# Kernel tuning notes

Hardware: AMD Instinct MI355X
Metric: run time of the kernel (lower is better)

## Reference

```python
import jax, jax.numpy as jnp
import numpy as np

B = 32768; SLOTS = 8; HEADS = 4; HEAD = 32; KEY = 32
MEM = HEADS * HEAD          # 128
QKV = 2 * KEY + HEAD        # 96 per head
TOT = HEADS * QKV           # 384
NGATE = 2 * MEM             # 256 (input + forget, unit gating)
FORGET_BIAS = 1.0; INPUT_BIAS = 0.0


def _ln(x, g, b, eps=1e-5):
    m = jnp.mean(x, axis=-1, keepdims=True)
    v = jnp.var(x, axis=-1, keepdims=True)
    return g * (x - m) * jax.lax.rsqrt(v + eps) + b


def setup_inputs():
    ks = jax.random.split(jax.random.key(0), 10)
    n = lambda k, shape, s=0.05: jax.random.normal(k, shape, dtype=jnp.float32) * s
    return {
        'inputs': jax.random.normal(ks[0], (B, MEM), dtype=jnp.float32),
        'memory': jax.random.normal(ks[1], (B, SLOTS, MEM), dtype=jnp.float32),
        'W_in': n(ks[2], (MEM, MEM)), 'b_in': jnp.zeros((MEM,), jnp.float32),
        'W_qkv': n(ks[3], (MEM, TOT)), 'b_qkv': jnp.zeros((TOT,), jnp.float32),
        'ln_qkv_g': jnp.ones((TOT,), jnp.float32), 'ln_qkv_b': jnp.zeros((TOT,), jnp.float32),
        'ln1_g': jnp.ones((MEM,), jnp.float32), 'ln1_b': jnp.zeros((MEM,), jnp.float32),
        'W_m1': n(ks[4], (MEM, MEM)), 'b_m1': jnp.zeros((MEM,), jnp.float32),
        'W_m2': n(ks[5], (MEM, MEM)), 'b_m2': jnp.zeros((MEM,), jnp.float32),
        'ln2_g': jnp.ones((MEM,), jnp.float32), 'ln2_b': jnp.zeros((MEM,), jnp.float32),
        'W_gi': n(ks[6], (MEM, NGATE)), 'b_gi': jnp.zeros((NGATE,), jnp.float32),
        'W_gm': n(ks[7], (MEM, NGATE)), 'b_gm': jnp.zeros((NGATE,), jnp.float32),
    }


def _forward(inputs, memory, W_in, b_in, W_qkv, b_qkv, ln_qkv_g, ln_qkv_b,
             ln1_g, ln1_b, W_m1, b_m1, W_m2, b_m2, ln2_g, ln2_b,
             W_gi, b_gi, W_gm, b_gm):
    x = inputs @ W_in + b_in                                  # [B, MEM]
    mp = jnp.concatenate([memory, x[:, None, :]], axis=1)     # [B, S1, MEM]
    S1 = SLOTS + 1
    # --- attend over memory (num_blocks = 1) ---
    qkv = _ln(mp @ W_qkv + b_qkv, ln_qkv_g, ln_qkv_b)         # [B, S1, TOT]
    qkv = qkv.reshape(-1, S1, HEADS, QKV).transpose(0, 2, 1, 3)  # [B, H, S1, QKV]
    q = qkv[..., :KEY] * (QKV ** -0.5)   # note: source scales by qkv_size, not key_size
    k = qkv[..., KEY:2 * KEY]
    v = qkv[..., 2 * KEY:]
    attn = jax.nn.softmax(jnp.einsum('bhqd,bhkd->bhqk', q, k), axis=-1)
    out = jnp.einsum('bhqk,bhkd->bhqd', attn, v)
    out = out.transpose(0, 2, 1, 3).reshape(-1, S1, MEM)      # [B, S1, MEM]
    mem = _ln(mp + out, ln1_g, ln1_b)
    mlp = (mem @ W_m1 + b_m1) @ W_m2 + b_m2   # stacked linears, no nonlinearity (as in source)
    mem = _ln(mlp + mem, ln2_g, ln2_b)
    next_mem = mem[:, :-1, :]                                 # drop input slot -> [B, SLOTS, MEM]
    # --- LSTM-style unit gating ---
    gi = x @ W_gi + b_gi                                      # [B, NGATE]
    gm = jnp.tanh(memory) @ W_gm + b_gm                       # [B, SLOTS, NGATE]
    gates = gm + gi[:, None, :]
    input_gate = jax.nn.sigmoid(gates[..., :MEM] + INPUT_BIAS)
    forget_gate = jax.nn.sigmoid(gates[..., MEM:] + FORGET_BIAS)
    next_mem = input_gate * jnp.tanh(next_mem) + forget_gate * memory
    output = next_mem.reshape(next_mem.shape[0], -1)          # [B, SLOTS*MEM]
    return output, next_mem


def reference(inputs, memory, W_in, b_in, W_qkv, b_qkv, ln_qkv_g, ln_qkv_b,
              ln1_g, ln1_b, W_m1, b_m1, W_m2, b_m2, ln2_g, ln2_b,
              W_gi, b_gi, W_gm, b_gm):
    return _forward(inputs, memory, W_in, b_in, W_qkv, b_qkv, ln_qkv_g, ln_qkv_b,
                    ln1_g, ln1_b, W_m1, b_m1, W_m2, b_m2, ln2_g, ln2_b,
                    W_gi, b_gi, W_gm, b_gm)
```

## Files before the change

kernel.cpp:

```cpp
#include <hip/hip_runtime.h>
#include <cstdint>
#include <cstddef>

#define BATCH   32768
#define BT      4
#define S1      9
#define RROWS   36
#define NBLK    (BATCH/BT)

#define WS_WIN   0
#define WS_WQKV  32768
#define WS_WC    131072
#define WS_WGI   163840
#define WS_WGM   229376
#define WS_BC    294912

#define A_OFF  27648
#define X_OFF  36864
#define MEM2   19456
#define LDSSZ  37888

typedef __bf16 bf16x8 __attribute__((ext_vector_type(8), may_alias));
typedef __bf16 bf16x4 __attribute__((ext_vector_type(4), may_alias));
typedef float  f32x4  __attribute__((ext_vector_type(4), may_alias));
typedef __bf16 bf16s  __attribute__((may_alias));
typedef float  f32s   __attribute__((may_alias));

__device__ __forceinline__ float sigmoidf_(float x){ return 1.f/(1.f+__expf(-x)); }
__device__ __forceinline__ float tanhf_(float x){ float e = __expf(2.f*x); return 1.f - 2.f/(e+1.f); }

__device__ __forceinline__ char* swz(char* base, int row, int stride, int colb){
  return base + row*stride + (colb ^ ((row & 7) << 4));
}

__global__ __launch_bounds__(256) void prep_kernel(
    const float* __restrict__ W_in,  const float* __restrict__ W_qkv,
    const float* __restrict__ W_m1,  const float* __restrict__ W_m2,
    const float* __restrict__ b_m1,  const float* __restrict__ b_m2,
    const float* __restrict__ W_gi,  const float* __restrict__ W_gm,
    __bf16* __restrict__ ws, float* __restrict__ bc)
{
  int gt = blockIdx.x*256 + threadIdx.x;
  int NT = gridDim.x*256;
  for (int i = gt; i < 128*128; i += NT){ int n=i>>7, k=i&127; ws[(WS_WIN >>1)+i] = (__bf16)W_in [k*128+n]; }
  for (int i = gt; i < 384*128; i += NT){ int n=i>>7, k=i&127; ws[(WS_WQKV>>1)+i] = (__bf16)W_qkv[k*384+n]; }
  for (int i = gt; i < 256*128; i += NT){ int n=i>>7, k=i&127; ws[(WS_WGI >>1)+i] = (__bf16)W_gi [k*256+n]; }
  for (int i = gt; i < 256*128; i += NT){ int n=i>>7, k=i&127; ws[(WS_WGM >>1)+i] = (__bf16)W_gm [k*256+n]; }
  for (int i = gt; i < 128*128; i += NT){
    int n=i>>7, k=i&127;
    float s = 0.f;
    for (int j=0;j<128;j++) s += W_m1[k*128+j]*W_m2[j*128+n];
    ws[(WS_WC>>1)+i] = (__bf16)s;
  }
  for (int i = gt; i < 128; i += NT){
    float s = b_m2[i];
    for (int j=0;j<128;j++) s += b_m1[j]*W_m2[j*128+i];
    bc[i] = s;
  }
}

__global__ __launch_bounds__(256, 4) void rmc_kernel(
    const float* __restrict__ inputs, const float* __restrict__ memory,
    const float* __restrict__ b_in,   const float* __restrict__ b_qkv,
    const float* __restrict__ lnq_g,  const float* __restrict__ lnq_b,
    const float* __restrict__ ln1_g,  const float* __restrict__ ln1_b,
    const float* __restrict__ ln2_g,  const float* __restrict__ ln2_b,
    const float* __restrict__ b_gi,   const float* __restrict__ b_gm,
    const __bf16* __restrict__ wWin,  const __bf16* __restrict__ wWqkv,
    const __bf16* __restrict__ wWc,   const __bf16* __restrict__ wWgi,
    const __bf16* __restrict__ wWgm,  const float* __restrict__ bc,
    float* __restrict__ out0, float* __restrict__ out1)
{
  __shared__ __align__(16) char smem[LDSSZ];
  char* Q = smem;
  char* A = smem + A_OFF;
  char* X = smem + X_OFF;

  const int tid  = threadIdx.x;
  const int lane = tid & 63;
  const int wv   = tid >> 6;
  const int l15  = lane & 15;
  const int lg   = lane >> 4;
  const int b0   = blockIdx.x * BT;
  const float QSC = 0.1020620726159658f;

  if (tid < 64){
    int r = tid >> 4, c = tid & 15;
    const float* gp = inputs + (size_t)(b0+r)*128 + c*8;
    f32x4 a = *(const f32x4*)gp, b = *(const f32x4*)(gp+4);
    bf16x8 h;
    h[0]=(__bf16)a[0]; h[1]=(__bf16)a[1]; h[2]=(__bf16)a[2]; h[3]=(__bf16)a[3];
    h[4]=(__bf16)b[0]; h[5]=(__bf16)b[1]; h[6]=(__bf16)b[2]; h[7]=(__bf16)b[3];
    *(bf16x8*)swz(X, r, 256, c*16) = h;
  }
  for (int t = tid; t < 512; t += 256){
    int r = t >> 4, c8 = (t & 15)*8;
    const float* gp = memory + (size_t)(b0 + (r>>3))*1024 + (r&7)*128 + c8;
    f32x4 a = *(const f32x4*)gp, b = *(const f32x4*)(gp+4);
    bf16x8 h;
    h[0]=(__bf16)a[0]; h[1]=(__bf16)a[1]; h[2]=(__bf16)a[2]; h[3]=(__bf16)a[3];
    h[4]=(__bf16)b[0]; h[5]=(__bf16)b[1]; h[6]=(__bf16)b[2]; h[7]=(__bf16)b[3];
    *(bf16x8*)swz(A, (r>>3)*S1 + (r&7), 256, c8*2) = h;
  }
  __syncthreads();

  {
    const int xr = (l15 < BT) ? l15 : (BT-1);
    bf16x8 aX[4];
#pragma unroll
    for (int k=0;k<4;k++) aX[k] = *(const bf16x8*)swz(X, xr, 256, k*64 + lg*16);
    f32x4 accX[2];
#pragma unroll
    for (int n=0;n<2;n++){
      int nt = wv*2 + n;
      f32x4 acc = {0.f,0.f,0.f,0.f};
#pragma unroll
      for (int k=0;k<4;k++){
        bf16x8 b = *(const bf16x8*)(wWin + (nt*16 + l15)*128 + k*32 + 8*lg);
        acc = __builtin_amdgcn_mfma_f32_16x16x32_bf16(aX[k], b, acc, 0, 0, 0);
      }
      accX[n] = acc;
    }
    __syncthreads();
#pragma unroll
    for (int n=0;n<2;n++){
#pragma unroll
      for (int r=0;r<4;r++){
        int row = 4*lg + r;
        if (row < BT){
          int col = (wv*2+n)*16 + l15;
          __bf16 h = (__bf16)(accX[n][r] + b_in[col]);
          *(bf16s*)swz(X, row, 256, col*2) = h;
          *(bf16s*)swz(A, row*S1+8, 256, col*2) = h;
        }
      }
    }
  }
  __syncthreads();

  {
    bf16x8 aQ[3][4];
#pragma unroll
    for (int m=0;m<3;m++){
      int ar = m*16 + l15; ar = (ar < RROWS) ? ar : (RROWS-1);
#pragma unroll
      for (int k=0;k<4;k++)
        aQ[m][k] = *(const bf16x8*)swz(A, ar, 256, k*64 + lg*16);
    }
#pragma unroll
    for (int half=0; half<2; ++half){
      f32x4 accQ[3][3];
#pragma unroll
      for (int m=0;m<3;m++)
#pragma unroll
        for (int n=0;n<3;n++) accQ[m][n] = (f32x4){0.f,0.f,0.f,0.f};
#pragma unroll
      for (int n=0;n<3;n++){
        int nt = wv*6 + half*3 + n;
#pragma unroll
        for (int k=0;k<4;k++){
          bf16x8 b = *(const bf16x8*)(wWqkv + (nt*16 + l15)*128 + k*32 + 8*lg);
#pragma unroll
          for (int m=0;m<3;m++)
            accQ[m][n] = __builtin_amdgcn_mfma_f32_16x16x32_bf16(aQ[m][k], b, accQ[m][n], 0, 0, 0);
        }
      }
#pragma unroll
      for (int m=0;m<3;m++)
#pragma unroll
        for (int n=0;n<3;n++)
#pragma unroll
          for (int r=0;r<4;r++){
            int row = m*16 + 4*lg + r;
            if (row < RROWS){
              int col = (wv*6 + half*3 + n)*16 + l15;
              *(bf16s*)swz(Q, row, 768, col*2) = (__bf16)(accQ[m][n][r] + b_qkv[col]);
            }
          }
    }
  }
  __syncthreads();

  {
    float gq[6], bq[6];
#pragma unroll
    for (int t=0;t<6;t++){ gq[t] = lnq_g[lane+64*t]; bq[t] = lnq_b[lane+64*t]; }
    for (int r = wv; r < RROWS; r += 4){
      float x[6]; float s = 0.f, sq = 0.f;
#pragma unroll
      for (int t=0;t<6;t++){
        x[t] = (float)*(const bf16s*)swz(Q, r, 768, (lane + 64*t)*2);
        s += x[t]; sq += x[t]*x[t];
      }
#pragma unroll
      for (int o=1;o<64;o<<=1){ s += __shfl_xor(s,o); sq += __shfl_xor(sq,o); }
      float mean = s * (1.f/384.f);
      float var  = sq * (1.f/384.f) - mean*mean;
      float rs   = rsqrtf(var + 1e-5f);
#pragma unroll
      for (int t=0;t<6;t++){
        int c = lane + 64*t;
        float y = gq[t]*(x[t]-mean)*rs + bq[t];
        if ((c % 96) < 32) y *= QSC;
        *(bf16s*)swz(Q, r, 768, c*2) = (__bf16)y;
      }
    }
  }
  __syncthreads();

  {
    const int s = wv;
    const int arow = (l15 < 9) ? l15 : 8;
    f32x4 sc[4];
#pragma unroll
    for (int h=0;h<4;h++){
      bf16x8 qa = *(const bf16x8*)swz(Q, s*S1+arow, 768, h*192 + lg*16);
      bf16x8 kb = *(const bf16x8*)swz(Q, s*S1+arow, 768, h*192 + 64 + lg*16);
      sc[h] = __builtin_amdgcn_mfma_f32_16x16x32_bf16(qa, kb, (f32x4){0.f,0.f,0.f,0.f}, 0, 0, 0);
    }
#pragma unroll
    for (int h=0;h<4;h++){
#pragma unroll
      for (int r=0;r<4;r++){
        int row = 4*lg + r;
        float v = (l15 < 9) ? sc[h][r] : -1e30f;
        float mx = v;
#pragma unroll
        for (int o=1;o<16;o<<=1) mx = fmaxf(mx, __shfl_xor(mx, o));
        float p = __expf(v - mx);
        float sm = p;
#pragma unroll
        for (int o=1;o<16;o<<=1) sm += __shfl_xor(sm, o);
        float pn = p / sm;
        if (row < 9 && l15 < 9)
          *(f32s*)swz(Q, s*S1+row, 768, h*192 + l15*4) = pn;
      }
    }
  }
  __syncthreads();

#pragma unroll
  for (int pass=0; pass<3; ++pass){
    int ct = pass*256 + tid;
    float o8[8] = {0.f,0.f,0.f,0.f,0.f,0.f,0.f,0.f};
    int s=0, h=0, q=0, d16=0;
    if (ct < 576){
      s = ct/144; int r2 = ct%144;
      h = r2/36;  int r3 = r2%36;
      q = r3>>2;  d16 = (r3&3)*16;
      int cb = h*192;
#pragma unroll
      for (int k=0;k<9;k++){
        float p = *(const f32s*)swz(Q, s*S1+q, 768, cb + k*4);
        bf16x8 v8 = *(const bf16x8*)swz(Q, s*S1+k, 768, cb + 128 + d16);
#pragma unroll
        for (int e=0;e<8;e++) o8[e] += p*(float)v8[e];
      }
    }
    __syncthreads();
    if (ct < 576){
      bf16x8 ho;
#pragma unroll
      for (int e=0;e<8;e++) ho[e] = (__bf16)o8[e];
      *(bf16x8*)swz(Q, s*S1+q, 768, h*192 + d16) = ho;
    }
    __syncthreads();
  }

  {
    float g0 = ln1_g[lane], g1 = ln1_g[lane+64], e0 = ln1_b[lane], e1 = ln1_b[lane+64];
    const int ob0 = (lane>>5)*192 + (lane&31)*2;
    const int ob1 = ((lane>>5)+2)*192 + (lane&31)*2;
    for (int r = wv; r < RROWS; r += 4){
      float t0 = (float)*(const bf16s*)swz(A, r, 256, lane*2)
               + (float)*(const bf16s*)swz(Q, r, 768, ob0);
      float t1 = (float)*(const bf16s*)swz(A, r, 256, (lane+64)*2)
               + (float)*(const bf16s*)swz(Q, r, 768, ob1);
      float s = t0+t1, sq = t0*t0 + t1*t1;
#pragma unroll
      for (int o=1;o<64;o<<=1){ s += __shfl_xor(s,o); sq += __shfl_xor(sq,o); }
      float mean = s*(1.f/128.f), var = sq*(1.f/128.f) - mean*mean;
      float rs = rsqrtf(var + 1e-5f);
      *(bf16s*)swz(A, r, 256, lane*2)      = (__bf16)(g0*(t0-mean)*rs + e0);
      *(bf16s*)swz(A, r, 256, (lane+64)*2) = (__bf16)(g1*(t1-mean)*rs + e1);
    }
  }
  __syncthreads();

  {
    bf16x8 aM[3][4];
#pragma unroll
    for (int m=0;m<3;m++){
      int ar = m*16 + l15; ar = (ar < RROWS) ? ar : (RROWS-1);
#pragma unroll
      for (int k=0;k<4;k++)
        aM[m][k] = *(const bf16x8*)swz(A, ar, 256, k*64 + lg*16);
    }
    f32x4 accM[3][2];
#pragma unroll
    for (int m=0;m<3;m++)
#pragma unroll
      for (int n=0;n<2;n++) accM[m][n] = (f32x4){0.f,0.f,0.f,0.f};
#pragma unroll
    for (int n=0;n<2;n++){
      int nt = wv*2 + n;
#pragma unroll
      for (int k=0;k<4;k++){
        bf16x8 b = *(const bf16x8*)(wWc + (nt*16 + l15)*128 + k*32 + 8*lg);
#pragma unroll
        for (int m=0;m<3;m++)
          accM[m][n] = __builtin_amdgcn_mfma_f32_16x16x32_bf16(aM[m][k], b, accM[m][n], 0, 0, 0);
      }
    }
    __syncthreads();
#pragma unroll
    for (int m=0;m<3;m++)
#pragma unroll
      for (int n=0;n<2;n++)
#pragma unroll
        for (int r=0;r<4;r++){
          int row = m*16 + 4*lg + r;
          if (row < RROWS){
            int col = (wv*2+n)*16 + l15;
            *(f32s*)swz(Q, row, 512, col*4) = accM[m][n][r] + bc[col];
          }
        }
  }
  __syncthreads();

  {
    float g0 = ln2_g[lane], g1 = ln2_g[lane+64], e0 = ln2_b[lane], e1 = ln2_b[lane+64];
    for (int r = wv; r < RROWS; r += 4){
      if ((r % S1) == 8) continue;
      float t0 = *(const f32s*)swz(Q, r, 512, lane*4)
               + (float)*(const bf16s*)swz(A, r, 256, lane*2);
      float t1 = *(const f32s*)swz(Q, r, 512, (lane+64)*4)
               + (float)*(const bf16s*)swz(A, r, 256, (lane+64)*2);
      float s = t0+t1, sq = t0*t0 + t1*t1;
#pragma unroll
      for (int o=1;o<64;o<<=1){ s += __shfl_xor(s,o); sq += __shfl_xor(sq,o); }
      float mean = s*(1.f/128.f), var = sq*(1.f/128.f) - mean*mean;
      float rs = rsqrtf(var + 1e-5f);
      int rp = (r/S1)*8 + (r%S1);
      *(bf16s*)swz(Q + MEM2, rp, 256, lane*2)      = (__bf16)(g0*(t0-mean)*rs + e0);
      *(bf16s*)swz(Q + MEM2, rp, 256, (lane+64)*2) = (__bf16)(g1*(t1-mean)*rs + e1);
    }
  }
  __syncthreads();

  {
    const int xr = (l15 < BT) ? l15 : (BT-1);
    bf16x8 aG[4];
#pragma unroll
    for (int k=0;k<4;k++) aG[k] = *(const bf16x8*)swz(X, xr, 256, k*64 + lg*16);
    f32x4 accG[4];
#pragma unroll
    for (int n=0;n<4;n++) accG[n] = (f32x4){0.f,0.f,0.f,0.f};
#pragma unroll
    for (int n=0;n<4;n++){
      int nt = wv*4 + n;
#pragma unroll
      for (int k=0;k<4;k++){
        bf16x8 b = *(const bf16x8*)(wWgi + (nt*16 + l15)*128 + k*32 + 8*lg);
        accG[n] = __builtin_amdgcn_mfma_f32_16x16x32_bf16(aG[k], b, accG[n], 0, 0, 0);
      }
    }
#pragma unroll
    for (int n=0;n<4;n++)
#pragma unroll
      for (int r=0;r<4;r++){
        int row = 4*lg + r;
        if (row < BT){
          int col = (wv*4+n)*16 + l15;
          *(f32s*)swz(Q, row, 1024, col*4) = accG[n][r] + b_gi[col];
        }
      }
    for (int t = tid; t < 512; t += 256){
      int r = t >> 4, c8 = (t & 15)*8;
      const float* gp = memory + (size_t)(b0 + (r>>3))*1024 + (r&7)*128 + c8;
      f32x4 a = *(const f32x4*)gp, b = *(const f32x4*)(gp+4);
      bf16x8 h;
      h[0]=(__bf16)tanhf_(a[0]); h[1]=(__bf16)tanhf_(a[1]);
      h[2]=(__bf16)tanhf_(a[2]); h[3]=(__bf16)tanhf_(a[3]);
      h[4]=(__bf16)tanhf_(b[0]); h[5]=(__bf16)tanhf_(b[1]);
      h[6]=(__bf16)tanhf_(b[2]); h[7]=(__bf16)tanhf_(b[3]);
      *(bf16x8*)swz(A, r, 256, c8*2) = h;
    }
  }
  __syncthreads();

  {
#pragma unroll
    for (int m=0;m<2;m++){
      bf16x8 aT[4];
#pragma unroll
      for (int k=0;k<4;k++)
        aT[k] = *(const bf16x8*)swz(A, m*16 + l15, 256, k*64 + lg*16);
#pragma unroll
      for (int p=0;p<2;p++){
        f32x4 ai = {0.f,0.f,0.f,0.f}, af = {0.f,0.f,0.f,0.f};
        int ntI = 2*wv + p, ntF = 8 + 2*wv + p;
#pragma unroll
        for (int k=0;k<4;k++){
          bf16x8 bI = *(const bf16x8*)(wWgm + (ntI*16 + l15)*128 + k*32 + 8*lg);
          bf16x8 bF = *(const bf16x8*)(wWgm + (ntF*16 + l15)*128 + k*32 + 8*lg);
          ai = __builtin_amdgcn_mfma_f32_16x16x32_bf16(aT[k], bI, ai, 0, 0, 0);
          af = __builtin_amdgcn_mfma_f32_16x16x32_bf16(aT[k], bF, af, 0, 0, 0);
        }
        int c = wv*32 + p*16 + l15;
        float giv = *(const f32s*)swz(Q, 0, 1024, 0) * 0.f;
        giv = *(const f32s*)swz(Q, 0, 1024, c*4);
        float bgi = b_gm[c], bgf = b_gm[128+c];
#pragma unroll
        for (int r=0;r<4;r++){
          int row = m*16 + 4*lg + r;
          int s = row>>3, j = row&7;
          float g_i = ai[r] + bgi + *(const f32s*)swz(Q, s, 1024, c*4);
          float g_f = af[r] + bgf + *(const f32s*)swz(Q, s, 1024, (128+c)*4) + 1.0f;
          float ig = sigmoidf_(g_i), fg = sigmoidf_(g_f);
          float m2 = (float)*(const bf16s*)swz(Q + MEM2, row, 256, c*2);
          float mo = memory[(size_t)(b0+s)*1024 + j*128 + c];
          float nm = ig*tanhf_(m2) + fg*mo;
          size_t o = (size_t)(b0+s)*1024 + (size_t)(j*128 + c);
          out0[o] = nm;
          out1[o] = nm;
        }
      }
    }
  }
}

extern "C" void kernel_launch(void* const* d_in, const int* in_sizes, int n_in,
                              void* d_out, int out_size, void* d_ws, size_t ws_size,
                              hipStream_t stream) {
  const float* inputs = (const float*)d_in[0];
  const float* memory = (const float*)d_in[1];
  const float* W_in   = (const float*)d_in[2];
  const float* b_in   = (const float*)d_in[3];
  const float* W_qkv  = (const float*)d_in[4];
  const float* b_qkv  = (const float*)d_in[5];
  const float* lnq_g  = (const float*)d_in[6];
  const float* lnq_b  = (const float*)d_in[7];
  const float* ln1_g  = (const float*)d_in[8];
  const float* ln1_b  = (const float*)d_in[9];
  const float* W_m1   = (const float*)d_in[10];
  const float* b_m1   = (const float*)d_in[11];
  const float* W_m2   = (const float*)d_in[12];
  const float* b_m2   = (const float*)d_in[13];
  const float* ln2_g  = (const float*)d_in[14];
  const float* ln2_b  = (const float*)d_in[15];
  const float* W_gi   = (const float*)d_in[16];
  const float* b_gi   = (const float*)d_in[17];
  const float* W_gm   = (const float*)d_in[18];
  const float* b_gm   = (const float*)d_in[19];

  __bf16* ws16 = (__bf16*)d_ws;
  float* bcp = (float*)((char*)d_ws + WS_BC);
  const __bf16* wWin  = (const __bf16*)((char*)d_ws + WS_WIN);
  const __bf16* wWqkv = (const __bf16*)((char*)d_ws + WS_WQKV);
  const __bf16* wWc   = (const __bf16*)((char*)d_ws + WS_WC);
  const __bf16* wWgi  = (const __bf16*)((char*)d_ws + WS_WGI);
  const __bf16* wWgm  = (const __bf16*)((char*)d_ws + WS_WGM);

  float* out0 = (float*)d_out;
  float* out1 = out0 + (size_t)BATCH*1024;

  prep_kernel<<<dim3(256), dim3(256), 0, stream>>>(
      W_in, W_qkv, W_m1, W_m2, b_m1, b_m2, W_gi, W_gm, ws16, bcp);

  rmc_kernel<<<dim3(NBLK), dim3(256), 0, stream>>>(
      inputs, memory, b_in, b_qkv, lnq_g, lnq_b, ln1_g, ln1_b, ln2_g, ln2_b,
      b_gi, b_gm, wWin, wWqkv, wWc, wWgi, wWgm, bcp, out0, out1);
}
```

Before: 563.2 us.

## Write attention output to unused Q region and process two rows per wave in LayerNorms

The attention-times-V stage now stores each output into the K column slot (cb+64) of its own row instead of overwriting the Q slot, so the three passes no longer need barriers between reading and writing. They collapse into one strided loop followed by a single barrier. Both LayerNorm stages now handle two rows per wave, one per 32-lane half, with 4 elements per lane and a 5-step shuffle reduction. The gamma and beta values are now fetched from global memory inside the loop. A dead shared-memory read in the gating stage is also removed.

```diff
diff --git a/kernel.cpp b/kernel.cpp
--- a/kernel.cpp
+++ b/kernel.cpp
@@ -239,50 +239,49 @@
   }
   __syncthreads();
 
-#pragma unroll
-  for (int pass=0; pass<3; ++pass){
-    int ct = pass*256 + tid;
+  for (int t = tid; t < 576; t += 256){
+    int s = t/144; int r2 = t%144;
+    int h = r2/36;  int r3 = r2%36;
+    int q = r3>>2;  int d16 = (r3&3)*16;
+    int cb = h*192;
     float o8[8] = {0.f,0.f,0.f,0.f,0.f,0.f,0.f,0.f};
-    int s=0, h=0, q=0, d16=0;
-    if (ct < 576){
-      s = ct/144; int r2 = ct%144;
-      h = r2/36;  int r3 = r2%36;
-      q = r3>>2;  d16 = (r3&3)*16;
-      int cb = h*192;
-#pragma unroll
-      for (int k=0;k<9;k++){
-        float p = *(const f32s*)swz(Q, s*S1+q, 768, cb + k*4);
-        bf16x8 v8 = *(const bf16x8*)swz(Q, s*S1+k, 768, cb + 128 + d16);
-#pragma unroll
-        for (int e=0;e<8;e++) o8[e] += p*(float)v8[e];
-      }
-    }
-    __syncthreads();
-    if (ct < 576){
-      bf16x8 ho;
-#pragma unroll
-      for (int e=0;e<8;e++) ho[e] = (__bf16)o8[e];
-      *(bf16x8*)swz(Q, s*S1+q, 768, h*192 + d16) = ho;
-    }
-    __syncthreads();
-  }
-
-  {
-    float g0 = ln1_g[lane], g1 = ln1_g[lane+64], e0 = ln1_b[lane], e1 = ln1_b[lane+64];
-    const int ob0 = (lane>>5)*192 + (lane&31)*2;
-    const int ob1 = ((lane>>5)+2)*192 + (lane&31)*2;
-    for (int r = wv; r < RROWS; r += 4){
-      float t0 = (float)*(const bf16s*)swz(A, r, 256, lane*2)
-               + (float)*(const bf16s*)swz(Q, r, 768, ob0);
-      float t1 = (float)*(const bf16s*)swz(A, r, 256, (lane+64)*2)
-               + (float)*(const bf16s*)swz(Q, r, 768, ob1);
-      float s = t0+t1, sq = t0*t0 + t1*t1;
-#pragma unroll
-      for (int o=1;o<64;o<<=1){ s += __shfl_xor(s,o); sq += __shfl_xor(sq,o); }
+#pragma unroll
+    for (int k=0;k<9;k++){
+      float p = *(const f32s*)swz(Q, s*S1+q, 768, cb + k*4);
+      bf16x8 v8 = *(const bf16x8*)swz(Q, s*S1+k, 768, cb + 128 + d16);
+#pragma unroll
+      for (int e=0;e<8;e++) o8[e] += p*(float)v8[e];
+    }
+    bf16x8 ho;
+#pragma unroll
+    for (int e=0;e<8;e++) ho[e] = (__bf16)o8[e];
+    *(bf16x8*)swz(Q, s*S1+q, 768, cb + 64 + d16) = ho;
+  }
+  __syncthreads();
+
+  {
+    const int half = lane >> 5;
+    const int l31  = lane & 31;
+    for (int base = wv*2; base < RROWS; base += 8){
+      int r = base + half;
+      float t[4]; float s = 0.f, sq = 0.f;
+#pragma unroll
+      for (int e=0;e<4;e++){
+        int c = l31 + 32*e;
+        float a = (float)*(const bf16s*)swz(A, r, 256, c*2)
+                + (float)*(const bf16s*)swz(Q, r, 768, e*192 + 64 + l31*2);
+        t[e] = a; s += a; sq += a*a;
+      }
+#pragma unroll
+      for (int o=1;o<32;o<<=1){ s += __shfl_xor(s,o); sq += __shfl_xor(sq,o); }
       float mean = s*(1.f/128.f), var = sq*(1.f/128.f) - mean*mean;
       float rs = rsqrtf(var + 1e-5f);
-      *(bf16s*)swz(A, r, 256, lane*2)      = (__bf16)(g0*(t0-mean)*rs + e0);
-      *(bf16s*)swz(A, r, 256, (lane+64)*2) = (__bf16)(g1*(t1-mean)*rs + e1);
+#pragma unroll
+      for (int e=0;e<4;e++){
+        int c = l31 + 32*e;
+        float y = ln1_g[c]*(t[e]-mean)*rs + ln1_b[c];
+        *(bf16s*)swz(A, r, 256, c*2) = (__bf16)y;
+      }
     }
   }
   __syncthreads();
@@ -329,21 +328,31 @@
   __syncthreads();
 
   {
-    float g0 = ln2_g[lane], g1 = ln2_g[lane+64], e0 = ln2_b[lane], e1 = ln2_b[lane+64];
-    for (int r = wv; r < RROWS; r += 4){
-      if ((r % S1) == 8) continue;
-      float t0 = *(const f32s*)swz(Q, r, 512, lane*4)
-               + (float)*(const bf16s*)swz(A, r, 256, lane*2);
-      float t1 = *(const f32s*)swz(Q, r, 512, (lane+64)*4)
-               + (float)*(const bf16s*)swz(A, r, 256, (lane+64)*2);
-      float s = t0+t1, sq = t0*t0 + t1*t1;
-#pragma unroll
-      for (int o=1;o<64;o<<=1){ s += __shfl_xor(s,o); sq += __shfl_xor(sq,o); }
-      float mean = s*(1.f/128.f), var = sq*(1.f/128.f) - mean*mean;
-      float rs = rsqrtf(var + 1e-5f);
-      int rp = (r/S1)*8 + (r%S1);
-      *(bf16s*)swz(Q + MEM2, rp, 256, lane*2)      = (__bf16)(g0*(t0-mean)*rs + e0);
-      *(bf16s*)swz(Q + MEM2, rp, 256, (lane+64)*2) = (__bf16)(g1*(t1-mean)*rs + e1);
+    const int half = lane >> 5;
+    const int l31  = lane & 31;
+    for (int base = wv*2; base < RROWS; base += 8){
+      int r = base + half;
+      if ((r % S1) != 8){
+        float t[4]; float s = 0.f, sq = 0.f;
+#pragma unroll
+        for (int e=0;e<4;e++){
+          int c = l31 + 32*e;
+          float a = *(const f32s*)swz(Q, r, 512, c*4)
+                  + (float)*(const bf16s*)swz(A, r, 256, c*2);
+          t[e] = a; s += a; sq += a*a;
+        }
+#pragma unroll
+        for (int o=1;o<32;o<<=1){ s += __shfl_xor(s,o); sq += __shfl_xor(sq,o); }
+        float mean = s*(1.f/128.f), var = sq*(1.f/128.f) - mean*mean;
+        float rs = rsqrtf(var + 1e-5f);
+        int rp = (r/S1)*8 + (r%S1);
+#pragma unroll
+        for (int e=0;e<4;e++){
+          int c = l31 + 32*e;
+          float y = ln2_g[c]*(t[e]-mean)*rs + ln2_b[c];
+          *(bf16s*)swz(Q + MEM2, rp, 256, c*2) = (__bf16)y;
+        }
+      }
     }
   }
   __syncthreads();
@@ -408,8 +417,6 @@
           af = __builtin_amdgcn_mfma_f32_16x16x32_bf16(aT[k], bF, af, 0, 0, 0);
         }
         int c = wv*32 + p*16 + l15;
-        float giv = *(const f32s*)swz(Q, 0, 1024, 0) * 0.f;
-        giv = *(const f32s*)swz(Q, 0, 1024, c*4);
         float bgi = b_gm[c], bgf = b_gm[128+c];
 #pragma unroll
         for (int r=0;r<4;r++){
```

New measurement: 552.2 us. About the same (-1.9%).
